# Kernel tuning notes

Hardware: AMD Instinct MI355X
Metric: run time of the kernel (lower is better)

Reference implementation:

```python
import jax, jax.numpy as jnp
import numpy as np

EPS = 1e-5


def _lin(k, fan_in, fan_out):
    return jax.random.normal(k, (fan_in, fan_out), jnp.float32) / np.sqrt(fan_in)


def setup_inputs() -> dict:
    key = jax.random.key(0)
    ks = jax.random.split(key, 12)
    N, E, F_in, H, G, S = 50000, 800000, 128, 64, 256, 64
    x = jax.random.normal(ks[0], (N, F_in), jnp.float32)
    edge_index = jax.random.randint(ks[1], (2, E), 0, N, dtype=jnp.int32)
    batch = jnp.sort(jax.random.randint(ks[2], (N,), 0, G, dtype=jnp.int32))
    sigma = jax.random.normal(ks[3], (G, S), jnp.float32)
    return {
        "x": x, "edge_index": edge_index, "batch": batch, "sigma": sigma,
        # GCN layers
        "W1": _lin(ks[4], F_in, H), "b1": jnp.zeros(H, jnp.float32),
        "g1": jnp.ones(H, jnp.float32), "be1": jnp.zeros(H, jnp.float32),
        "W2": _lin(ks[5], H, H), "b2": jnp.zeros(H, jnp.float32),
        "g2": jnp.ones(H, jnp.float32), "be2": jnp.zeros(H, jnp.float32),
        "W3": _lin(ks[6], H, H), "b3": jnp.zeros(H, jnp.float32),
        "g3": jnp.ones(H, jnp.float32), "be3": jnp.zeros(H, jnp.float32),
        # feed-forward branch
        "Wf1": _lin(ks[7], S, 2 * H), "bf1": jnp.zeros(2 * H, jnp.float32),
        "Wf2": _lin(ks[8], 2 * H, H), "bf2": jnp.zeros(H, jnp.float32),
        # fusion head
        "Wfu": _lin(ks[9], 2 * H, 1), "bfu": jnp.zeros(1, jnp.float32),
    }


def _gcn(x, W, b, src, dst, dis, N):
    """PyG GCNConv: D^-1/2 (A+I) D^-1/2 X W + b, with self-loops."""
    h = x @ W                                        # [N, H]
    norm = (dis[src] * dis[dst])[:, None]            # [E, 1]
    agg = jax.ops.segment_sum(h[src] * norm, dst, num_segments=N)
    agg = agg + h * (dis * dis)[:, None]             # self-loop contribution
    return agg + b


def _bn(x, g, be):
    mu = x.mean(axis=0)
    var = x.var(axis=0)  # biased, matches torch BN normalization
    return (x - mu) * jax.lax.rsqrt(var + EPS) * g + be


def reference(x, edge_index, batch, sigma,
              W1, b1, g1, be1, W2, b2, g2, be2, W3, b3, g3, be3,
              Wf1, bf1, Wf2, bf2, Wfu, bfu):
    N = x.shape[0]
    G = sigma.shape[0]
    src, dst = edge_index[0], edge_index[1]
    # symmetric normalization with self-loops: deg = 1 + in-degree
    deg = jax.ops.segment_sum(jnp.ones(src.shape[0], x.dtype), dst, num_segments=N) + 1.0
    dis = jax.lax.rsqrt(deg)

    h = jax.nn.relu(_bn(_gcn(x, W1, b1, src, dst, dis, N), g1, be1))
    h_res = h
    h = jax.nn.relu(_bn(_gcn(h, W2, b2, src, dst, dis, N), g2, be2) + h_res)
    h = jax.nn.relu(_bn(_gcn(h, W3, b3, src, dst, dis, N), g3, be3))

    # global mean pool over graphs
    sums = jax.ops.segment_sum(h, batch, num_segments=G)
    cnt = jax.ops.segment_sum(jnp.ones(N, x.dtype), batch, num_segments=G)
    gcn_emb = sums / jnp.maximum(cnt, 1.0)[:, None]   # [G, H]

    # feed-forward branch (dropout off in eval)
    f = jax.nn.relu(sigma @ Wf1 + bf1)
    f = jax.nn.relu(f @ Wf2 + bf2)                    # [G, H]

    fused = jnp.concatenate([gcn_emb, f], axis=1)     # [G, 2H]
    out = fused @ Wfu + bfu
    return out.squeeze(-1)                            # [G]
```

## Files before the change

kernel.cpp:

```cpp
#include <hip/hip_runtime.h>
#include <hip/hip_bf16.h>

__device__ __forceinline__ float b2f(unsigned short u) {
    union { unsigned int i; float f; } t; t.i = ((unsigned int)u) << 16; return t.f;
}

__global__ void k_hist(const int* __restrict__ dst, int* __restrict__ cnt, int E) {
    int e = blockIdx.x * blockDim.x + threadIdx.x;
    if (e < E) atomicAdd(&cnt[dst[e]], 1);
}

__global__ void k_scanA(const int* __restrict__ cnt, int* __restrict__ bsum, int N) {
    __shared__ int sh[256];
    int i = blockIdx.x * 256 + threadIdx.x;
    sh[threadIdx.x] = (i < N) ? cnt[i] : 0;
    __syncthreads();
    for (int off = 128; off > 0; off >>= 1) {
        if (threadIdx.x < off) sh[threadIdx.x] += sh[threadIdx.x + off];
        __syncthreads();
    }
    if (threadIdx.x == 0) bsum[blockIdx.x] = sh[0];
}

__global__ void k_scanB(int* __restrict__ bsum, int nb) {
    __shared__ int sh[1024];
    int t = threadIdx.x;
    sh[t] = (t < nb) ? bsum[t] : 0;
    __syncthreads();
    for (int off = 1; off < 1024; off <<= 1) {
        int v = (t >= off) ? sh[t - off] : 0;
        __syncthreads();
        sh[t] += v;
        __syncthreads();
    }
    if (t < nb) bsum[t] = (t == 0) ? 0 : sh[t - 1];
}

__global__ void k_scanC(const int* __restrict__ cnt, const int* __restrict__ boff,
                        int* __restrict__ row_ptr, int4* __restrict__ rc4,
                        float* __restrict__ dis, int N) {
    __shared__ int sh[256];
    int i = blockIdx.x * 256 + threadIdx.x;
    int v = (i < N) ? cnt[i] : 0;
    sh[threadIdx.x] = v;
    __syncthreads();
    for (int off = 1; off < 256; off <<= 1) {
        int u = (threadIdx.x >= off) ? sh[threadIdx.x - off] : 0;
        __syncthreads();
        sh[threadIdx.x] += u;
        __syncthreads();
    }
    if (i < N) {
        int start = sh[threadIdx.x] - v + boff[blockIdx.x];
        float d = rsqrtf((float)v + 1.0f);
        row_ptr[i] = start;
        rc4[i] = make_int4(start, v, __float_as_int(d), 0);
        dis[i] = d;
    }
}

__global__ void k_fill(const int* __restrict__ src, const int* __restrict__ dst,
                       const int* __restrict__ row_ptr, int* __restrict__ cursor,
                       int* __restrict__ csr_src, int E) {
    int e = blockIdx.x * blockDim.x + threadIdx.x;
    if (e < E) {
        int d = dst[e];
        int pos = row_ptr[d] + atomicAdd(&cursor[d], 1);
        csr_src[pos] = src[e];
    }
}

template <int K>
__global__ void __launch_bounds__(256, 4) k_gemm_lds(const float* __restrict__ in,
                                                     const float* __restrict__ W,
                                                     const float* __restrict__ dis,
                                                     __hip_bfloat16* __restrict__ out,
                                                     int N) {
    constexpr int KF = K / 4;
    __shared__ float Wl[K * 64];
    __shared__ float4 xt[16 * KF];
    __shared__ float dl[16];
    for (int i = threadIdx.x; i < K * 16; i += 256)
        ((float4*)Wl)[i] = ((const float4*)W)[i];
    int col = threadIdx.x & 63;
    int rg  = threadIdx.x >> 6;
    const float4* in4 = (const float4*)in;
    const float4 zero4 = {0.f, 0.f, 0.f, 0.f};
    int ntiles = (N + 15) >> 4;
    for (int t = blockIdx.x; t < ntiles; t += gridDim.x) {
        int base = t * 16;
        __syncthreads();
        for (int i = threadIdx.x; i < 16 * KF; i += 256) {
            int r = i / KF, f = i - r * KF;
            int row = base + r;
            xt[i] = (row < N) ? in4[(size_t)row * KF + f] : zero4;
        }
        if (threadIdx.x < 16) {
            int row = base + threadIdx.x;
            dl[threadIdx.x] = (row < N) ? dis[row] : 0.f;
        }
        __syncthreads();
        float acc0 = 0.f, acc1 = 0.f, acc2 = 0.f, acc3 = 0.f;
#pragma unroll 2
        for (int kg = 0; kg < KF; ++kg) {
            float w0 = Wl[(4 * kg + 0) * 64 + col];
            float w1 = Wl[(4 * kg + 1) * 64 + col];
            float w2 = Wl[(4 * kg + 2) * 64 + col];
            float w3 = Wl[(4 * kg + 3) * 64 + col];
            float4 x0 = xt[(rg * 4 + 0) * KF + kg];
            float4 x1 = xt[(rg * 4 + 1) * KF + kg];
            float4 x2 = xt[(rg * 4 + 2) * KF + kg];
            float4 x3 = xt[(rg * 4 + 3) * KF + kg];
            acc0 = fmaf(x0.w, w3, fmaf(x0.z, w2, fmaf(x0.y, w1, fmaf(x0.x, w0, acc0))));
            acc1 = fmaf(x1.w, w3, fmaf(x1.z, w2, fmaf(x1.y, w1, fmaf(x1.x, w0, acc1))));
            acc2 = fmaf(x2.w, w3, fmaf(x2.z, w2, fmaf(x2.y, w1, fmaf(x2.x, w0, acc2))));
            acc3 = fmaf(x3.w, w3, fmaf(x3.z, w2, fmaf(x3.y, w1, fmaf(x3.x, w0, acc3))));
        }
        int r0 = base + rg * 4;
        if (r0 + 3 < N) {
            out[(size_t)(r0 + 0) * 64 + col] = __float2bfloat16(acc0 * dl[rg * 4 + 0]);
            out[(size_t)(r0 + 1) * 64 + col] = __float2bfloat16(acc1 * dl[rg * 4 + 1]);
            out[(size_t)(r0 + 2) * 64 + col] = __float2bfloat16(acc2 * dl[rg * 4 + 2]);
            out[(size_t)(r0 + 3) * 64 + col] = __float2bfloat16(acc3 * dl[rg * 4 + 3]);
        } else {
            if (r0 + 0 < N) out[(size_t)(r0 + 0) * 64 + col] = __float2bfloat16(acc0 * dl[rg * 4 + 0]);
            if (r0 + 1 < N) out[(size_t)(r0 + 1) * 64 + col] = __float2bfloat16(acc1 * dl[rg * 4 + 1]);
            if (r0 + 2 < N) out[(size_t)(r0 + 2) * 64 + col] = __float2bfloat16(acc2 * dl[rg * 4 + 2]);
            if (r0 + 3 < N) out[(size_t)(r0 + 3) * 64 + col] = __float2bfloat16(acc3 * dl[rg * 4 + 3]);
        }
    }
}

__global__ void __launch_bounds__(256) k_gather8v2(const int4* __restrict__ rc4,
                                                   const int* __restrict__ csr_src,
                                                   const __hip_bfloat16* __restrict__ hs,
                                                   const float* __restrict__ b,
                                                   float* __restrict__ z,
                                                   float* __restrict__ stats, int N) {
    const unsigned short* hsu = (const unsigned short*)hs;
    int tid  = threadIdx.x;
    int lane = tid & 63;
    int w    = tid >> 6;
    int grp  = lane >> 3;
    int sub  = lane & 7;
    float vb[8];
    *(float4*)&vb[0] = *(const float4*)(b + sub * 8);
    *(float4*)&vb[4] = *(const float4*)(b + sub * 8 + 4);
    float ps[8] = {0,0,0,0,0,0,0,0}, pq[8] = {0,0,0,0,0,0,0,0};
    int wid = blockIdx.x * 4 + w;
    int nw  = gridDim.x * 4;
    const float4 zero4 = {0.f, 0.f, 0.f, 0.f};
    for (int base = wid * 2; base < N; base += nw * 2) {
        int nA = base;
        int nB = base + 1;
        bool hasB = (nB < N);
        int4 ra = rc4[nA];
        int4 rb = hasB ? rc4[nB] : make_int4(0, 0, 0, 0);
        int startA = ra.x, cA = ra.y; float dA = __int_as_float(ra.z);
        int startB = rb.x, cB = rb.y; float dB = __int_as_float(rb.z);
        int sA0 = -1, sA1 = -1, sA2 = -1, sB0 = -1, sB1 = -1, sB2 = -1;
        if (grp      < cA) sA0 = csr_src[startA + grp];
        if (8 + grp  < cA) sA1 = csr_src[startA + 8 + grp];
        if (16 + grp < cA) sA2 = csr_src[startA + 16 + grp];
        if (grp      < cB) sB0 = csr_src[startB + grp];
        if (8 + grp  < cB) sB1 = csr_src[startB + 8 + grp];
        if (16 + grp < cB) sB2 = csr_src[startB + 16 + grp];
        float4 rA0 = zero4, rA1 = zero4, rA2 = zero4;
        float4 rB0 = zero4, rB1 = zero4, rB2 = zero4;
        if (sA0 >= 0) rA0 = *(const float4*)(hsu + (size_t)sA0 * 64 + sub * 8);
        if (sA1 >= 0) rA1 = *(const float4*)(hsu + (size_t)sA1 * 64 + sub * 8);
        if (sA2 >= 0) rA2 = *(const float4*)(hsu + (size_t)sA2 * 64 + sub * 8);
        if (sB0 >= 0) rB0 = *(const float4*)(hsu + (size_t)sB0 * 64 + sub * 8);
        if (sB1 >= 0) rB1 = *(const float4*)(hsu + (size_t)sB1 * 64 + sub * 8);
        if (sB2 >= 0) rB2 = *(const float4*)(hsu + (size_t)sB2 * 64 + sub * 8);
        float4 selfA = *(const float4*)(hsu + (size_t)nA * 64 + sub * 8);
        float4 selfB = hasB ? *(const float4*)(hsu + (size_t)nB * 64 + sub * 8) : zero4;
        float accA[8], accB[8];
        {
            const unsigned short* uA0 = (const unsigned short*)&rA0;
            const unsigned short* uA1 = (const unsigned short*)&rA1;
            const unsigned short* uA2 = (const unsigned short*)&rA2;
            const unsigned short* uB0 = (const unsigned short*)&rB0;
            const unsigned short* uB1 = (const unsigned short*)&rB1;
            const unsigned short* uB2 = (const unsigned short*)&rB2;
#pragma unroll
            for (int i = 0; i < 8; ++i) {
                accA[i] = b2f(uA0[i]) + b2f(uA1[i]) + b2f(uA2[i]);
                accB[i] = b2f(uB0[i]) + b2f(uB1[i]) + b2f(uB2[i]);
            }
        }
        for (int j = 24; j + grp < cA; j += 8) {
            int s = csr_src[startA + j + grp];
            float4 raw = *(const float4*)(hsu + (size_t)s * 64 + sub * 8);
            const unsigned short* us = (const unsigned short*)&raw;
#pragma unroll
            for (int i = 0; i < 8; ++i) accA[i] += b2f(us[i]);
        }
        for (int j = 24; j + grp < cB; j += 8) {
            int s = csr_src[startB + j + grp];
            float4 raw = *(const float4*)(hsu + (size_t)s * 64 + sub * 8);
            const unsigned short* us = (const unsigned short*)&raw;
#pragma unroll
            for (int i = 0; i < 8; ++i) accB[i] += b2f(us[i]);
        }
#pragma unroll
        for (int i = 0; i < 8; ++i) { accA[i] += __shfl_xor(accA[i], 8);  accB[i] += __shfl_xor(accB[i], 8); }
#pragma unroll
        for (int i = 0; i < 8; ++i) { accA[i] += __shfl_xor(accA[i], 16); accB[i] += __shfl_xor(accB[i], 16); }
#pragma unroll
        for (int i = 0; i < 8; ++i) { accA[i] += __shfl_xor(accA[i], 32); accB[i] += __shfl_xor(accB[i], 32); }
        if (grp == 0) {
            const unsigned short* suA = (const unsigned short*)&selfA;
            float v[8];
#pragma unroll
            for (int i = 0; i < 8; ++i) {
                v[i] = (accA[i] + b2f(suA[i])) * dA + vb[i];
                ps[i] += v[i];
                pq[i] += v[i] * v[i];
            }
            *(float4*)(z + (size_t)nA * 64 + sub * 8)     = *(float4*)&v[0];
            *(float4*)(z + (size_t)nA * 64 + sub * 8 + 4) = *(float4*)&v[4];
            if (hasB) {
                const unsigned short* suB = (const unsigned short*)&selfB;
#pragma unroll
                for (int i = 0; i < 8; ++i) {
                    v[i] = (accB[i] + b2f(suB[i])) * dB + vb[i];
                    ps[i] += v[i];
                    pq[i] += v[i] * v[i];
                }
                *(float4*)(z + (size_t)nB * 64 + sub * 8)     = *(float4*)&v[0];
                *(float4*)(z + (size_t)nB * 64 + sub * 8 + 4) = *(float4*)&v[4];
            }
        }
    }
    __shared__ float ssum[4][64], ssq[4][64];
    if (grp == 0) {
        *(float4*)&ssum[w][sub * 8]     = *(float4*)&ps[0];
        *(float4*)&ssum[w][sub * 8 + 4] = *(float4*)&ps[4];
        *(float4*)&ssq[w][sub * 8]      = *(float4*)&pq[0];
        *(float4*)&ssq[w][sub * 8 + 4]  = *(float4*)&pq[4];
    }
    __syncthreads();
    if (tid < 64) {
        float s = ssum[0][tid] + ssum[1][tid] + ssum[2][tid] + ssum[3][tid];
        float q = ssq[0][tid] + ssq[1][tid] + ssq[2][tid] + ssq[3][tid];
        atomicAdd(&stats[tid], s);
        atomicAdd(&stats[64 + tid], q);
    }
}

__global__ void k_norm4(const float* __restrict__ z, const float* __restrict__ stats,
                        const float* __restrict__ g, const float* __restrict__ be,
                        const float* __restrict__ res, float* __restrict__ out,
                        float invN, int total4) {
    int i = blockIdx.x * blockDim.x + threadIdx.x;
    if (i >= total4) return;
    int cb = (i & 15) * 4;
    float4 zv = ((const float4*)z)[i];
    float v[4] = {zv.x, zv.y, zv.z, zv.w};
#pragma unroll
    for (int k = 0; k < 4; ++k) {
        int c = cb + k;
        float mu  = stats[c] * invN;
        float var = stats[64 + c] * invN - mu * mu;
        float sc  = g[c] * rsqrtf(var + 1e-5f);
        float sh  = be[c] - mu * sc;
        v[k] = v[k] * sc + sh;
    }
    if (res) {
        float4 rv = ((const float4*)res)[i];
        v[0] += rv.x; v[1] += rv.y; v[2] += rv.z; v[3] += rv.w;
    }
    float4 o;
    o.x = fmaxf(v[0], 0.f); o.y = fmaxf(v[1], 0.f);
    o.z = fmaxf(v[2], 0.f); o.w = fmaxf(v[3], 0.f);
    ((float4*)out)[i] = o;
}

__global__ void k_norm_pool(const float* __restrict__ z, const float* __restrict__ stats,
                            const float* __restrict__ g, const float* __restrict__ be,
                            const int* __restrict__ batch, float* __restrict__ psums,
                            float* __restrict__ pcnt, float invN, int N, int per) {
    int lane = threadIdx.x & 63;
    int wave = (blockIdx.x * blockDim.x + threadIdx.x) >> 6;
    int begin = wave * per;
    if (begin >= N) return;
    int end = begin + per; if (end > N) end = N;
    float mu  = stats[lane] * invN;
    float var = stats[64 + lane] * invN - mu * mu;
    float sc  = g[lane] * rsqrtf(var + 1e-5f);
    float sh  = be[lane] - mu * sc;
    int   cur = batch[begin];
    float run = 0.f;
    int   crun = 0;
    for (int n = begin; n < end; ++n) {
        int gg = batch[n];
        if (gg != cur) {
            atomicAdd(&psums[(size_t)cur * 64 + lane], run);
            if (lane == 0) atomicAdd(&pcnt[cur], (float)crun);
            run = 0.f; crun = 0; cur = gg;
        }
        float v = fmaxf(z[(size_t)n * 64 + lane] * sc + sh, 0.f);
        run += v; crun++;
    }
    atomicAdd(&psums[(size_t)cur * 64 + lane], run);
    if (lane == 0) atomicAdd(&pcnt[cur], (float)crun);
}

__global__ void k_head(const float* __restrict__ sigma, const float* __restrict__ Wf1,
                       const float* __restrict__ bf1, const float* __restrict__ Wf2,
                       const float* __restrict__ bf2, const float* __restrict__ Wfu,
                       const float* __restrict__ bfu, const float* __restrict__ sums,
                       const float* __restrict__ cnt, float* __restrict__ out) {
    int g = blockIdx.x;
    int t = threadIdx.x;
    __shared__ float srow[64], f1[128], f2[64];
    if (t < 64) srow[t] = sigma[(size_t)g * 64 + t];
    __syncthreads();
    {
        float acc = bf1[t];
        for (int s = 0; s < 64; ++s) acc += srow[s] * Wf1[s * 128 + t];
        f1[t] = fmaxf(acc, 0.f);
    }
    __syncthreads();
    if (t < 64) {
        float a2 = bf2[t];
        for (int k = 0; k < 128; ++k) a2 += f1[k] * Wf2[k * 64 + t];
        f2[t] = fmaxf(a2, 0.f);
    }
    __syncthreads();
    if (t < 64) {
        float inv    = 1.0f / fmaxf(cnt[g], 1.0f);
        float pooled = sums[(size_t)g * 64 + t] * inv;
        float contrib = pooled * Wfu[t] + f2[t] * Wfu[64 + t];
#pragma unroll
        for (int o = 32; o > 0; o >>= 1) contrib += __shfl_down(contrib, o);
        if (t == 0) out[g] = contrib + bfu[0];
    }
}

extern "C" void kernel_launch(void* const* d_in, const int* in_sizes, int n_in,
                              void* d_out, int out_size, void* d_ws, size_t ws_size,
                              hipStream_t stream) {
    const float* x     = (const float*)d_in[0];
    const int*   ei    = (const int*)d_in[1];
    const int*   batch = (const int*)d_in[2];
    const float* sigma = (const float*)d_in[3];
    const float* W1 = (const float*)d_in[4];  const float* b1 = (const float*)d_in[5];
    const float* g1 = (const float*)d_in[6];  const float* be1 = (const float*)d_in[7];
    const float* W2 = (const float*)d_in[8];  const float* b2 = (const float*)d_in[9];
    const float* g2 = (const float*)d_in[10]; const float* be2 = (const float*)d_in[11];
    const float* W3 = (const float*)d_in[12]; const float* b3 = (const float*)d_in[13];
    const float* g3 = (const float*)d_in[14]; const float* be3 = (const float*)d_in[15];
    const float* Wf1 = (const float*)d_in[16]; const float* bf1 = (const float*)d_in[17];
    const float* Wf2 = (const float*)d_in[18]; const float* bf2 = (const float*)d_in[19];
    const float* Wfu = (const float*)d_in[20]; const float* bfu = (const float*)d_in[21];

    const int N = in_sizes[0] / 128;
    const int E = in_sizes[1] / 2;
    const int G = in_sizes[3] / 64;
    const int* src = ei;
    const int* dst = ei + E;

    float* ws   = (float*)d_ws;
    float* bufA = ws;
    float* bufB = bufA + (size_t)N * 64;
    float* bufC = bufB + (size_t)N * 64;
    __hip_bfloat16* hsb = (__hip_bfloat16*)(bufC + (size_t)N * 64);
    float* dis  = (float*)(hsb + (size_t)N * 64);
    int4*  rc4     = (int4*)(dis + N);
    int*   row_ptr = (int*)(rc4 + N);
    int*   bsum    = row_ptr + N;
    int*   csr_src = bsum + 1024;
    int*   cnt     = csr_src + E;
    int*   cursor  = cnt + N;
    float* stats1  = (float*)(cursor + N);
    float* stats2  = stats1 + 128;
    float* stats3  = stats2 + 128;
    float* psums   = stats3 + 128;
    float* pcnt    = psums + (size_t)G * 64;
    size_t zero_bytes = ((char*)(pcnt + G)) - ((char*)cnt);

    const float invN = 1.0f / (float)N;
    const int totNH  = N * 64;
    const int tot4   = totNH / 4;
    const int nb     = (N + 255) / 256;

    hipMemsetAsync(cnt, 0, zero_bytes, stream);

    k_hist<<<(E + 255) / 256, 256, 0, stream>>>(dst, cnt, E);
    k_scanA<<<nb, 256, 0, stream>>>(cnt, bsum, N);
    k_scanB<<<1, 1024, 0, stream>>>(bsum, nb);
    k_scanC<<<nb, 256, 0, stream>>>(cnt, bsum, row_ptr, rc4, dis, N);
    k_fill<<<(E + 255) / 256, 256, 0, stream>>>(src, dst, row_ptr, cursor, csr_src, E);

    k_gemm_lds<128><<<1024, 256, 0, stream>>>(x, W1, dis, hsb, N);
    k_gather8v2<<<2048, 256, 0, stream>>>(rc4, csr_src, hsb, b1, bufB, stats1, N);
    k_norm4<<<(tot4 + 255) / 256, 256, 0, stream>>>(bufB, stats1, g1, be1, nullptr, bufC, invN, tot4);

    k_gemm_lds<64><<<1024, 256, 0, stream>>>(bufC, W2, dis, hsb, N);
    k_gather8v2<<<2048, 256, 0, stream>>>(rc4, csr_src, hsb, b2, bufA, stats2, N);
    k_norm4<<<(tot4 + 255) / 256, 256, 0, stream>>>(bufA, stats2, g2, be2, bufC, bufB, invN, tot4);

    k_gemm_lds<64><<<1024, 256, 0, stream>>>(bufB, W3, dis, hsb, N);
    k_gather8v2<<<2048, 256, 0, stream>>>(rc4, csr_src, hsb, b3, bufA, stats3, N);

    {
        const int waves = 8192;
        int per = (N + waves - 1) / waves;
        k_norm_pool<<<2048, 256, 0, stream>>>(bufA, stats3, g3, be3, batch, psums, pcnt, invN, N, per);
    }

    k_head<<<G, 128, 0, stream>>>(sigma, Wf1, bf1, Wf2, bf2, Wfu, bfu, psums, pcnt, (float*)d_out);
}
```

Measured before the change: 393.9 us.

## Fuse batchnorm+ReLU+residual into next layer's GEMM load; nontemporal gather I/O

The two standalone normalize kernels are removed. Each GEMM now computes BN scale and shift from the accumulated stats and applies BN, residual and ReLU while staging input rows into LDS. Layer 3 recomputes layer 1's normalized activation from its raw pre-BN buffer instead of reading a stored residual. Separately, the gather kernel uses nontemporal loads for CSR indices and nontemporal stores for its output. This saves two launches and two full N×64 read/write passes, at the cost of extra ALU work and an extra input read in the third GEMM.

```diff
diff --git a/kernel.cpp b/kernel.cpp
--- a/kernel.cpp
+++ b/kernel.cpp
@@ -1,5 +1,7 @@
 #include <hip/hip_runtime.h>
 #include <hip/hip_bf16.h>
+
+typedef float f32x4 __attribute__((ext_vector_type(4)));
 
 __device__ __forceinline__ float b2f(unsigned short u) {
     union { unsigned int i; float f; } t; t.i = ((unsigned int)u) << 16; return t.f;
@@ -70,21 +72,48 @@
     }
 }
 
-template <int K>
+template <int K, int MODE>
 __global__ void __launch_bounds__(256, 4) k_gemm_lds(const float* __restrict__ in,
+                                                     const float* __restrict__ in2,
                                                      const float* __restrict__ W,
                                                      const float* __restrict__ dis,
+                                                     const float* __restrict__ statsB,
+                                                     const float* __restrict__ gB,
+                                                     const float* __restrict__ beB,
+                                                     const float* __restrict__ statsA,
+                                                     const float* __restrict__ gA,
+                                                     const float* __restrict__ beA,
                                                      __hip_bfloat16* __restrict__ out,
-                                                     int N) {
+                                                     float invN, int N) {
     constexpr int KF = K / 4;
     __shared__ float Wl[K * 64];
     __shared__ float4 xt[16 * KF];
     __shared__ float dl[16];
+    __shared__ float scb[64], shb[64], sca[64], sha[64];
     for (int i = threadIdx.x; i < K * 16; i += 256)
         ((float4*)Wl)[i] = ((const float4*)W)[i];
+    if constexpr (MODE >= 1) {
+        if (threadIdx.x < 64) {
+            int c = threadIdx.x;
+            float mu  = statsB[c] * invN;
+            float var = statsB[64 + c] * invN - mu * mu;
+            float s   = gB[c] * rsqrtf(var + 1e-5f);
+            scb[c] = s; shb[c] = beB[c] - mu * s;
+        }
+    }
+    if constexpr (MODE == 2) {
+        if (threadIdx.x >= 64 && threadIdx.x < 128) {
+            int c = threadIdx.x - 64;
+            float mu  = statsA[c] * invN;
+            float var = statsA[64 + c] * invN - mu * mu;
+            float s   = gA[c] * rsqrtf(var + 1e-5f);
+            sca[c] = s; sha[c] = beA[c] - mu * s;
+        }
+    }
     int col = threadIdx.x & 63;
     int rg  = threadIdx.x >> 6;
-    const float4* in4 = (const float4*)in;
+    const float4* in4  = (const float4*)in;
+    const float4* in24 = (const float4*)in2;
     const float4 zero4 = {0.f, 0.f, 0.f, 0.f};
     int ntiles = (N + 15) >> 4;
     for (int t = blockIdx.x; t < ntiles; t += gridDim.x) {
@@ -93,7 +122,29 @@
         for (int i = threadIdx.x; i < 16 * KF; i += 256) {
             int r = i / KF, f = i - r * KF;
             int row = base + r;
-            xt[i] = (row < N) ? in4[(size_t)row * KF + f] : zero4;
+            float4 v = zero4;
+            if (row < N) {
+                v = in4[(size_t)row * KF + f];
+                if constexpr (MODE >= 1) {
+                    float4 sc = ((const float4*)scb)[f];
+                    float4 sh = ((const float4*)shb)[f];
+                    float rx = 0.f, ry = 0.f, rz = 0.f, rw = 0.f;
+                    if constexpr (MODE == 2) {
+                        float4 u  = in24[(size_t)row * KF + f];
+                        float4 sa = ((const float4*)sca)[f];
+                        float4 ha = ((const float4*)sha)[f];
+                        rx = fmaxf(u.x * sa.x + ha.x, 0.f);
+                        ry = fmaxf(u.y * sa.y + ha.y, 0.f);
+                        rz = fmaxf(u.z * sa.z + ha.z, 0.f);
+                        rw = fmaxf(u.w * sa.w + ha.w, 0.f);
+                    }
+                    v.x = fmaxf(v.x * sc.x + sh.x + rx, 0.f);
+                    v.y = fmaxf(v.y * sc.y + sh.y + ry, 0.f);
+                    v.z = fmaxf(v.z * sc.z + sh.z + rz, 0.f);
+                    v.w = fmaxf(v.w * sc.w + sh.w + rw, 0.f);
+                }
+            }
+            xt[i] = v;
         }
         if (threadIdx.x < 16) {
             int row = base + threadIdx.x;
@@ -159,12 +210,12 @@
         int startA = ra.x, cA = ra.y; float dA = __int_as_float(ra.z);
         int startB = rb.x, cB = rb.y; float dB = __int_as_float(rb.z);
         int sA0 = -1, sA1 = -1, sA2 = -1, sB0 = -1, sB1 = -1, sB2 = -1;
-        if (grp      < cA) sA0 = csr_src[startA + grp];
-        if (8 + grp  < cA) sA1 = csr_src[startA + 8 + grp];
-        if (16 + grp < cA) sA2 = csr_src[startA + 16 + grp];
-        if (grp      < cB) sB0 = csr_src[startB + grp];
-        if (8 + grp  < cB) sB1 = csr_src[startB + 8 + grp];
-        if (16 + grp < cB) sB2 = csr_src[startB + 16 + grp];
+        if (grp      < cA) sA0 = __builtin_nontemporal_load(&csr_src[startA + grp]);
+        if (8 + grp  < cA) sA1 = __builtin_nontemporal_load(&csr_src[startA + 8 + grp]);
+        if (16 + grp < cA) sA2 = __builtin_nontemporal_load(&csr_src[startA + 16 + grp]);
+        if (grp      < cB) sB0 = __builtin_nontemporal_load(&csr_src[startB + grp]);
+        if (8 + grp  < cB) sB1 = __builtin_nontemporal_load(&csr_src[startB + 8 + grp]);
+        if (16 + grp < cB) sB2 = __builtin_nontemporal_load(&csr_src[startB + 16 + grp]);
         float4 rA0 = zero4, rA1 = zero4, rA2 = zero4;
         float4 rB0 = zero4, rB1 = zero4, rB2 = zero4;
         if (sA0 >= 0) rA0 = *(const float4*)(hsu + (size_t)sA0 * 64 + sub * 8);
@@ -218,8 +269,8 @@
                 ps[i] += v[i];
                 pq[i] += v[i] * v[i];
             }
-            *(float4*)(z + (size_t)nA * 64 + sub * 8)     = *(float4*)&v[0];
-            *(float4*)(z + (size_t)nA * 64 + sub * 8 + 4) = *(float4*)&v[4];
+            __builtin_nontemporal_store(*(f32x4*)&v[0], (f32x4*)(z + (size_t)nA * 64 + sub * 8));
+            __builtin_nontemporal_store(*(f32x4*)&v[4], (f32x4*)(z + (size_t)nA * 64 + sub * 8 + 4));
             if (hasB) {
                 const unsigned short* suB = (const unsigned short*)&selfB;
 #pragma unroll
@@ -228,8 +279,8 @@
                     ps[i] += v[i];
                     pq[i] += v[i] * v[i];
                 }
-                *(float4*)(z + (size_t)nB * 64 + sub * 8)     = *(float4*)&v[0];
-                *(float4*)(z + (size_t)nB * 64 + sub * 8 + 4) = *(float4*)&v[4];
+                __builtin_nontemporal_store(*(f32x4*)&v[0], (f32x4*)(z + (size_t)nB * 64 + sub * 8));
+                __builtin_nontemporal_store(*(f32x4*)&v[4], (f32x4*)(z + (size_t)nB * 64 + sub * 8 + 4));
             }
         }
     }
@@ -247,34 +298,6 @@
         atomicAdd(&stats[tid], s);
         atomicAdd(&stats[64 + tid], q);
     }
-}
-
-__global__ void k_norm4(const float* __restrict__ z, const float* __restrict__ stats,
-                        const float* __restrict__ g, const float* __restrict__ be,
-                        const float* __restrict__ res, float* __restrict__ out,
-                        float invN, int total4) {
-    int i = blockIdx.x * blockDim.x + threadIdx.x;
-    if (i >= total4) return;
-    int cb = (i & 15) * 4;
-    float4 zv = ((const float4*)z)[i];
-    float v[4] = {zv.x, zv.y, zv.z, zv.w};
-#pragma unroll
-    for (int k = 0; k < 4; ++k) {
-        int c = cb + k;
-        float mu  = stats[c] * invN;
-        float var = stats[64 + c] * invN - mu * mu;
-        float sc  = g[c] * rsqrtf(var + 1e-5f);
-        float sh  = be[c] - mu * sc;
-        v[k] = v[k] * sc + sh;
-    }
-    if (res) {
-        float4 rv = ((const float4*)res)[i];
-        v[0] += rv.x; v[1] += rv.y; v[2] += rv.z; v[3] += rv.w;
-    }
-    float4 o;
-    o.x = fmaxf(v[0], 0.f); o.y = fmaxf(v[1], 0.f);
-    o.z = fmaxf(v[2], 0.f); o.w = fmaxf(v[3], 0.f);
-    ((float4*)out)[i] = o;
 }
 
 __global__ void k_norm_pool(const float* __restrict__ z, const float* __restrict__ stats,
@@ -382,8 +405,6 @@
     size_t zero_bytes = ((char*)(pcnt + G)) - ((char*)cnt);
 
     const float invN = 1.0f / (float)N;
-    const int totNH  = N * 64;
-    const int tot4   = totNH / 4;
     const int nb     = (N + 255) / 256;
 
     hipMemsetAsync(cnt, 0, zero_bytes, stream);
@@ -394,21 +415,22 @@
     k_scanC<<<nb, 256, 0, stream>>>(cnt, bsum, row_ptr, rc4, dis, N);
     k_fill<<<(E + 255) / 256, 256, 0, stream>>>(src, dst, row_ptr, cursor, csr_src, E);
 
-    k_gemm_lds<128><<<1024, 256, 0, stream>>>(x, W1, dis, hsb, N);
+    k_gemm_lds<128, 0><<<1024, 256, 0, stream>>>(x, nullptr, W1, dis,
+        nullptr, nullptr, nullptr, nullptr, nullptr, nullptr, hsb, invN, N);
     k_gather8v2<<<2048, 256, 0, stream>>>(rc4, csr_src, hsb, b1, bufB, stats1, N);
-    k_norm4<<<(tot4 + 255) / 256, 256, 0, stream>>>(bufB, stats1, g1, be1, nullptr, bufC, invN, tot4);
-
-    k_gemm_lds<64><<<1024, 256, 0, stream>>>(bufC, W2, dis, hsb, N);
+
+    k_gemm_lds<64, 1><<<1024, 256, 0, stream>>>(bufB, nullptr, W2, dis,
+        stats1, g1, be1, nullptr, nullptr, nullptr, hsb, invN, N);
     k_gather8v2<<<2048, 256, 0, stream>>>(rc4, csr_src, hsb, b2, bufA, stats2, N);
-    k_norm4<<<(tot4 + 255) / 256, 256, 0, stream>>>(bufA, stats2, g2, be2, bufC, bufB, invN, tot4);
-
-    k_gemm_lds<64><<<1024, 256, 0, stream>>>(bufB, W3, dis, hsb, N);
-    k_gather8v2<<<2048, 256, 0, stream>>>(rc4, csr_src, hsb, b3, bufA, stats3, N);
+
+    k_gemm_lds<64, 2><<<1024, 256, 0, stream>>>(bufA, bufB, W3, dis,
+        stats2, g2, be2, stats1, g1, be1, hsb, invN, N);
+    k_gather8v2<<<2048, 256, 0, stream>>>(rc4, csr_src, hsb, b3, bufC, stats3, N);
 
     {
         const int waves = 8192;
         int per = (N + waves - 1) / waves;
-        k_norm_pool<<<2048, 256, 0, stream>>>(bufA, stats3, g3, be3, batch, psums, pcnt, invN, N, per);
+        k_norm_pool<<<2048, 256, 0, stream>>>(bufC, stats3, g3, be3, batch, psums, pcnt, invN, N, per);
     }
 
     k_head<<<G, 128, 0, stream>>>(sigma, Wf1, bf1, Wf2, bf2, Wfu, bfu, psums, pcnt, (float*)d_out);
```

Result: no change. 387.6 us (-1.6%).
